# Kernel optimization log

Hardware: AMD Instinct MI355X
Metric: run time of the kernel (lower is better)

The kernel has to match this reference:

```python
import jax, jax.numpy as jnp
import numpy as np

B, T, D = 64, 2048, 256  # batch, seq_len, embedding_dim; units == embedding_dim == D
U = 256


def setup_inputs() -> dict:
    key = jax.random.key(0)
    ks = jax.random.split(key, 8)
    s = 1.0 / np.sqrt(D)
    return {
        "features": jax.random.normal(ks[0], (B, T, D), dtype=jnp.float32),
        "hidden": jax.random.normal(ks[1], (B, D), dtype=jnp.float32),
        "w1_w": jax.random.uniform(ks[2], (U, D), jnp.float32, -s, s),
        "w1_b": jax.random.uniform(ks[3], (U,), jnp.float32, -s, s),
        "w2_w": jax.random.uniform(ks[4], (U, D), jnp.float32, -s, s),
        "w2_b": jax.random.uniform(ks[5], (U,), jnp.float32, -s, s),
        "v_w": jax.random.uniform(ks[6], (1, U), jnp.float32, -s, s),
        "v_b": jax.random.uniform(ks[7], (1,), jnp.float32, -s, s),
    }


def reference(features, hidden, w1_w, w1_b, w2_w, w2_b, v_w, v_b):
    # features: [B, T, D], hidden: [B, D]
    proj = jnp.einsum('btd,ud->btu', features, w1_w) + w1_b  # w1(features)
    hid = jnp.einsum('bd,ud->bu', hidden, w2_w) + w2_b        # w2(hidden)
    score = jnp.einsum('btu,ou->bto', jnp.tanh(proj + hid[:, None, :]), v_w) + v_b  # [B,T,1]
    attn = jax.nn.softmax(score, axis=1)                      # [B,T,1]
    context = jnp.sum(attn * features, axis=1)                # [B,D]
    return context, attn
```

## Files before the change

### kernel.cpp

```cpp
#include <hip/hip_runtime.h>
#include <stdint.h>

#define Bq 64
#define Tq 2048
#define Dq 256
#define Uq 256
#define NTILE 32

typedef __bf16 bf16x8 __attribute__((ext_vector_type(8)));
typedef float f32x4 __attribute__((ext_vector_type(4)));

#define ASTR 1024
#define ABUF (4 * ASTR)
#define BSTR 4096
#define BBUF (4 * BSTR)

__device__ inline unsigned short rne_bf16(float a) {
  unsigned b = __float_as_uint(a);
  return (unsigned short)((b + 0x7FFFu + ((b >> 16) & 1u)) >> 16);
}

__device__ inline float fast_tanh(float x) {
  float e = __expf(2.0f * x);
  return 1.0f - 2.0f * __builtin_amdgcn_rcpf(e + 1.0f);
}

__global__ void k01_prep(const float* __restrict__ w1,
                         unsigned short* __restrict__ w1bf,
                         const float* __restrict__ hidden,
                         const float* __restrict__ w2_w,
                         const float* __restrict__ w2_b,
                         const float* __restrict__ w1_b,
                         float* __restrict__ comb) {
  if (blockIdx.x < 64) {
    int idx = blockIdx.x * 256 + threadIdx.x;
    int i = idx * 4;
    int u = i >> 8;
    int k = i & 255;
    float4 v = *reinterpret_cast<const float4*>(&w1[i]);
    ushort4 h;
    h.x = rne_bf16(v.x);
    h.y = rne_bf16(v.y);
    h.z = rne_bf16(v.z);
    h.w = rne_bf16(v.w);
    int dst = (k >> 3) * (Uq * 8) + u * 8 + (k & 7);
    *reinterpret_cast<ushort4*>(&w1bf[dst]) = h;
  } else {
    int bid = blockIdx.x - 64;
    int b = bid >> 6;
    int wave = threadIdx.x >> 6;
    int lane = threadIdx.x & 63;
    int u = (bid & 63) * 4 + wave;
    const float* h = hidden + b * Dq;
    const float* w = w2_w + u * Dq;
    float sum = 0.f;
#pragma unroll
    for (int i = 0; i < Dq; i += 64) sum += h[lane + i] * w[lane + i];
#pragma unroll
    for (int m = 32; m >= 1; m >>= 1) sum += __shfl_xor(sum, m, 64);
    if (lane == 0) comb[b * Uq + u] = sum + w2_b[u] + w1_b[u];
  }
}

__global__ __launch_bounds__(256) void k2_score(
    const float* __restrict__ feat, const unsigned short* __restrict__ w1bf,
    const float* __restrict__ comb, const float* __restrict__ v_w,
    const float* __restrict__ v_b, float* __restrict__ score,
    float* __restrict__ pm, float* __restrict__ partc) {
  __shared__ char sB[2 * BBUF];
  __shared__ char sA[2 * ABUF];
  float* const scp = reinterpret_cast<float*>(sA);
  float* const ebuf = reinterpret_cast<float*>(sA) + 256;
  const int b = blockIdx.y;
  const int tile = blockIdx.x;
  const int t0 = tile * 64;
  const int tid = threadIdx.x;
  const int w = tid >> 6;
  const int l = tid & 63;
  const int fr = l & 15;
  const int g = l >> 4;

  const int arow = tid >> 2;
  const int aoct = tid & 3;
  const float* aload = feat + ((size_t)(b * Tq + t0 + arow)) * Dq + aoct * 8;
  char* const awr = sA + aoct * ASTR + arow * 16;

  f32x4 acc[4][4] = {};
  float4 pa[2][2];

  auto issueBdma = [&](int c) {
    char* bbase = sB + (c & 1) * BBUF;
#pragma unroll
    for (int q = 0; q < 4; ++q) {
      int d = w * 4 + q;
      int j = d >> 2;
      int h2 = d & 3;
      const unsigned short* src =
          w1bf + (size_t)(c * 4 + j) * (Uq * 8) + (h2 * 64 + l) * 8;
      __builtin_amdgcn_global_load_lds(
          (const __attribute__((address_space(1))) unsigned int*)src,
          (__attribute__((address_space(3))) unsigned int*)(bbase + j * BSTR +
                                                            h2 * 1024),
          16, 0, 0);
    }
  };
  auto loadA = [&](int c) {
    pa[c & 1][0] = *reinterpret_cast<const float4*>(aload + c * 32);
    pa[c & 1][1] = *reinterpret_cast<const float4*>(aload + c * 32 + 4);
  };
  auto writeA = [&](int c) {
    const float4& v0 = pa[c & 1][0];
    const float4& v1 = pa[c & 1][1];
    uint4 H;
    H.x = rne_bf16(v0.x) | ((unsigned)rne_bf16(v0.y) << 16);
    H.y = rne_bf16(v0.z) | ((unsigned)rne_bf16(v0.w) << 16);
    H.z = rne_bf16(v1.x) | ((unsigned)rne_bf16(v1.y) << 16);
    H.w = rne_bf16(v1.z) | ((unsigned)rne_bf16(v1.w) << 16);
    *reinterpret_cast<uint4*>(awr + (c & 1) * ABUF) = H;
  };
  auto pipeBarrier = [&]() {
    __builtin_amdgcn_sched_barrier(0);
    asm volatile("s_waitcnt vmcnt(2) lgkmcnt(0)" ::: "memory");
    __builtin_amdgcn_s_barrier();
    __builtin_amdgcn_sched_barrier(0);
  };

  issueBdma(0);
  __builtin_amdgcn_sched_barrier(0);
  loadA(0);
  loadA(1);
  __builtin_amdgcn_sched_barrier(0);
  writeA(0);
  pipeBarrier();

#pragma unroll
  for (int c = 0; c < 8; ++c) {
    if (c < 7) {
      issueBdma(c + 1);
      __builtin_amdgcn_sched_barrier(0);
      loadA((c + 2) & 7);
      __builtin_amdgcn_sched_barrier(0);
    }
    const char* bA = sA + (c & 1) * ABUF;
    const char* bB = sB + (c & 1) * BBUF;
    bf16x8 ah[4], bh[4];
#pragma unroll
    for (int mf = 0; mf < 4; ++mf)
      ah[mf] = *reinterpret_cast<const bf16x8*>(bA + g * ASTR +
                                                (mf * 16 + fr) * 16);
#pragma unroll
    for (int nf = 0; nf < 4; ++nf)
      bh[nf] = *reinterpret_cast<const bf16x8*>(
          bB + g * BSTR + (w * 64 + nf * 16 + fr) * 16);
    __builtin_amdgcn_s_setprio(1);
#pragma unroll
    for (int mf = 0; mf < 4; ++mf)
#pragma unroll
      for (int nf = 0; nf < 4; ++nf)
        acc[mf][nf] = __builtin_amdgcn_mfma_f32_16x16x32_bf16(
            ah[mf], bh[nf], acc[mf][nf], 0, 0, 0);
    __builtin_amdgcn_s_setprio(0);
    if (c < 7) {
      writeA(c + 1);
      pipeBarrier();
    }
  }

  const float* frow = feat + (size_t)(b * Tq + t0) * Dq + tid;
  float fv0[16], fv1[16];
#pragma unroll
  for (int t = 0; t < 16; ++t) fv0[t] = frow[(size_t)t * Dq];
#pragma unroll
  for (int t = 0; t < 16; ++t) fv1[t] = frow[(size_t)(t + 16) * Dq];

  float cb[4], vw4[4];
#pragma unroll
  for (int nf = 0; nf < 4; ++nf) {
    int u = w * 64 + nf * 16 + fr;
    cb[nf] = comb[b * Uq + u];
    vw4[nf] = v_w[u];
  }
  float sc[4][4];
#pragma unroll
  for (int mf = 0; mf < 4; ++mf)
#pragma unroll
    for (int r = 0; r < 4; ++r) sc[mf][r] = 0.f;
#pragma unroll
  for (int mf = 0; mf < 4; ++mf)
#pragma unroll
    for (int nf = 0; nf < 4; ++nf)
#pragma unroll
      for (int r = 0; r < 4; ++r)
        sc[mf][r] += vw4[nf] * fast_tanh(acc[mf][nf][r] + cb[nf]);
#pragma unroll
  for (int m = 1; m < 16; m <<= 1)
#pragma unroll
    for (int mf = 0; mf < 4; ++mf)
#pragma unroll
      for (int r = 0; r < 4; ++r) sc[mf][r] += __shfl_xor(sc[mf][r], m, 16);
  __syncthreads();
  if (fr == 0) {
#pragma unroll
    for (int mf = 0; mf < 4; ++mf)
#pragma unroll
      for (int r = 0; r < 4; ++r)
        scp[w * 64 + mf * 16 + g * 4 + r] = sc[mf][r];
  }
  __syncthreads();
  if (tid < 64) {
    float v =
        scp[tid] + scp[64 + tid] + scp[128 + tid] + scp[192 + tid] + v_b[0];
    score[b * Tq + t0 + tid] = v;
    float m = v;
#pragma unroll
    for (int mk = 32; mk >= 1; mk >>= 1) m = fmaxf(m, __shfl_xor(m, mk, 64));
    ebuf[tid] = __expf(v - m);
    if (tid == 0) pm[b * NTILE + tile] = m;
  }
  __syncthreads();
  {
    float fv2[16], fv3[16];
#pragma unroll
    for (int t = 0; t < 16; ++t) fv2[t] = frow[(size_t)(t + 32) * Dq];
    float cd = 0.f;
#pragma unroll
    for (int t = 0; t < 16; ++t) cd += ebuf[t] * fv0[t];
#pragma unroll
    for (int t = 0; t < 16; ++t) fv3[t] = frow[(size_t)(t + 48) * Dq];
#pragma unroll
    for (int t = 0; t < 16; ++t) cd += ebuf[t + 16] * fv1[t];
#pragma unroll
    for (int t = 0; t < 16; ++t) cd += ebuf[t + 32] * fv2[t];
#pragma unroll
    for (int t = 0; t < 16; ++t) cd += ebuf[t + 48] * fv3[t];
    partc[((size_t)b * NTILE + tile) * Dq + tid] = cd;
  }
}

__global__ void k35_softmax_combine(float* __restrict__ s,
                                    const float* __restrict__ pm,
                                    const float* __restrict__ partc,
                                    float* __restrict__ ctx) {
  int b = blockIdx.x;
  int tid = threadIdx.x;
  const int base = b * Tq;
  float v[8];
  float m = -1e30f;
#pragma unroll
  for (int i = 0; i < 8; ++i) {
    v[i] = s[base + tid + 256 * i];
    m = fmaxf(m, v[i]);
  }
#pragma unroll
  for (int mk = 32; mk >= 1; mk >>= 1) m = fmaxf(m, __shfl_xor(m, mk, 64));
  __shared__ float red[4];
  int wv = tid >> 6, ln = tid & 63;
  if (ln == 0) red[wv] = m;
  __syncthreads();
  m = fmaxf(fmaxf(red[0], red[1]), fmaxf(red[2], red[3]));
  __syncthreads();
  float sum = 0.f;
#pragma unroll
  for (int i = 0; i < 8; ++i) {
    v[i] = __expf(v[i] - m);
    sum += v[i];
  }
#pragma unroll
  for (int mk = 32; mk >= 1; mk >>= 1) sum += __shfl_xor(sum, mk, 64);
  if (ln == 0) red[wv] = sum;
  __syncthreads();
  sum = red[0] + red[1] + red[2] + red[3];
  float inv = 1.f / sum;
#pragma unroll
  for (int i = 0; i < 8; ++i) s[base + tid + 256 * i] = v[i] * inv;

  __shared__ float wgt[NTILE];
  if (tid < NTILE) wgt[tid] = __expf(pm[b * NTILE + tid] - m);
  __syncthreads();
  float cs = 0.f;
#pragma unroll
  for (int j = 0; j < NTILE; ++j)
    cs += wgt[j] * partc[((size_t)b * NTILE + j) * Dq + tid];
  ctx[b * Dq + tid] = cs * inv;
}

extern "C" void kernel_launch(void* const* d_in, const int* in_sizes, int n_in,
                              void* d_out, int out_size, void* d_ws,
                              size_t ws_size, hipStream_t stream) {
  const float* feat   = (const float*)d_in[0];
  const float* hidden = (const float*)d_in[1];
  const float* w1_w   = (const float*)d_in[2];
  const float* w1_b   = (const float*)d_in[3];
  const float* w2_w   = (const float*)d_in[4];
  const float* w2_b   = (const float*)d_in[5];
  const float* v_w    = (const float*)d_in[6];
  const float* v_b    = (const float*)d_in[7];

  float* ctx  = (float*)d_out;
  float* attn = ctx + Bq * Dq;
  float* comb = (float*)d_ws;
  unsigned short* w1bf = (unsigned short*)(comb + Bq * Uq);
  float* partc = (float*)(w1bf + Uq * Dq);
  float* pm    = partc + (size_t)Bq * NTILE * Dq;

  k01_prep<<<64 + Bq * 64, 256, 0, stream>>>(w1_w, w1bf, hidden, w2_w, w2_b,
                                             w1_b, comb);
  k2_score<<<dim3(NTILE, Bq), 256, 0, stream>>>(feat, w1bf, comb, v_w, v_b,
                                                attn, pm, partc);
  k35_softmax_combine<<<Bq, 256, 0, stream>>>(attn, pm, partc, ctx);
}
```

Measured before the change: 61.76 us.

## Double score-kernel row tile to 128 with 512 threads sharing W1 tiles

Each block of the score kernel now covers 128 time steps instead of 64. It uses 8 waves in a 2x4 layout, so each bf16 W1 chunk staged in LDS serves two row groups, halving W1 reloads per token, and the grid shrinks to 16 tiles per batch. The A-tile LDS stride is padded to 2080 bytes, likely to reduce bank conflicts. The block-wide softmax max and the context partials are now combined across two halves through extra shared-memory reductions and barriers, which adds sync overhead and register pressure at 512 threads.

Result: slower. 65.63 us (+6.3%).

```diff
diff --git a/kernel.cpp b/kernel.cpp
--- a/kernel.cpp
+++ b/kernel.cpp
@@ -5,13 +5,13 @@
 #define Tq 2048
 #define Dq 256
 #define Uq 256
-#define NTILE 32
+#define NTILE 16
 
 typedef __bf16 bf16x8 __attribute__((ext_vector_type(8)));
 typedef float f32x4 __attribute__((ext_vector_type(4)));
 
-#define ASTR 1024
-#define ABUF (4 * ASTR)
+#define AOST 2080
+#define ABUF (4 * AOST)
 #define BSTR 4096
 #define BBUF (4 * BSTR)
 
@@ -62,7 +62,7 @@
   }
 }
 
-__global__ __launch_bounds__(256) void k2_score(
+__global__ __launch_bounds__(512) void k2_score(
     const float* __restrict__ feat, const unsigned short* __restrict__ w1bf,
     const float* __restrict__ comb, const float* __restrict__ v_w,
     const float* __restrict__ v_b, float* __restrict__ score,
@@ -70,20 +70,24 @@
   __shared__ char sB[2 * BBUF];
   __shared__ char sA[2 * ABUF];
   float* const scp = reinterpret_cast<float*>(sA);
-  float* const ebuf = reinterpret_cast<float*>(sA) + 256;
+  float* const ebuf = reinterpret_cast<float*>(sA) + 512;
+  float* const red = reinterpret_cast<float*>(sA) + 640;
+  float* const cbuf = reinterpret_cast<float*>(sA) + 644;
   const int b = blockIdx.y;
   const int tile = blockIdx.x;
-  const int t0 = tile * 64;
+  const int t0 = tile * 128;
   const int tid = threadIdx.x;
   const int w = tid >> 6;
   const int l = tid & 63;
   const int fr = l & 15;
   const int g = l >> 4;
+  const int wr = w >> 2;
+  const int wc = w & 3;
 
   const int arow = tid >> 2;
   const int aoct = tid & 3;
   const float* aload = feat + ((size_t)(b * Tq + t0 + arow)) * Dq + aoct * 8;
-  char* const awr = sA + aoct * ASTR + arow * 16;
+  char* const awr = sA + aoct * AOST + arow * 16;
 
   f32x4 acc[4][4] = {};
   float4 pa[2][2];
@@ -91,8 +95,8 @@
   auto issueBdma = [&](int c) {
     char* bbase = sB + (c & 1) * BBUF;
 #pragma unroll
-    for (int q = 0; q < 4; ++q) {
-      int d = w * 4 + q;
+    for (int q = 0; q < 2; ++q) {
+      int d = w * 2 + q;
       int j = d >> 2;
       int h2 = d & 3;
       const unsigned short* src =
@@ -146,12 +150,12 @@
     bf16x8 ah[4], bh[4];
 #pragma unroll
     for (int mf = 0; mf < 4; ++mf)
-      ah[mf] = *reinterpret_cast<const bf16x8*>(bA + g * ASTR +
-                                                (mf * 16 + fr) * 16);
+      ah[mf] = *reinterpret_cast<const bf16x8*>(
+          bA + g * AOST + (wr * 64 + mf * 16 + fr) * 16);
 #pragma unroll
     for (int nf = 0; nf < 4; ++nf)
       bh[nf] = *reinterpret_cast<const bf16x8*>(
-          bB + g * BSTR + (w * 64 + nf * 16 + fr) * 16);
+          bB + g * BSTR + (wc * 64 + nf * 16 + fr) * 16);
     __builtin_amdgcn_s_setprio(1);
 #pragma unroll
     for (int mf = 0; mf < 4; ++mf)
@@ -166,7 +170,10 @@
     }
   }
 
-  const float* frow = feat + (size_t)(b * Tq + t0) * Dq + tid;
+  const int cd_ = tid & 255;
+  const int th = tid >> 8;
+  const float* frow =
+      feat + ((size_t)(b * Tq + t0 + th * 64)) * Dq + cd_;
   float fv0[16], fv1[16];
 #pragma unroll
   for (int t = 0; t < 16; ++t) fv0[t] = frow[(size_t)t * Dq];
@@ -176,7 +183,7 @@
   float cb[4], vw4[4];
 #pragma unroll
   for (int nf = 0; nf < 4; ++nf) {
-    int u = w * 64 + nf * 16 + fr;
+    int u = wc * 64 + nf * 16 + fr;
     cb[nf] = comb[b * Uq + u];
     vw4[nf] = v_w[u];
   }
@@ -204,36 +211,44 @@
     for (int mf = 0; mf < 4; ++mf)
 #pragma unroll
       for (int r = 0; r < 4; ++r)
-        scp[w * 64 + mf * 16 + g * 4 + r] = sc[mf][r];
-  }
-  __syncthreads();
-  if (tid < 64) {
-    float v =
-        scp[tid] + scp[64 + tid] + scp[128 + tid] + scp[192 + tid] + v_b[0];
+        scp[wc * 128 + wr * 64 + mf * 16 + g * 4 + r] = sc[mf][r];
+  }
+  __syncthreads();
+  float v = 0.f;
+  if (tid < 128) {
+    v = scp[tid] + scp[128 + tid] + scp[256 + tid] + scp[384 + tid] + v_b[0];
     score[b * Tq + t0 + tid] = v;
-    float m = v;
-#pragma unroll
-    for (int mk = 32; mk >= 1; mk >>= 1) m = fmaxf(m, __shfl_xor(m, mk, 64));
-    ebuf[tid] = __expf(v - m);
-    if (tid == 0) pm[b * NTILE + tile] = m;
-  }
+    float mloc = v;
+#pragma unroll
+    for (int mk = 32; mk >= 1; mk >>= 1)
+      mloc = fmaxf(mloc, __shfl_xor(mloc, mk, 64));
+    if ((tid & 63) == 0) red[tid >> 6] = mloc;
+  }
+  __syncthreads();
+  const float mb = fmaxf(red[0], red[1]);
+  if (tid < 128) ebuf[tid] = __expf(v - mb);
+  if (tid == 0) pm[b * NTILE + tile] = mb;
   __syncthreads();
   {
+    const float* eb = ebuf + th * 64;
     float fv2[16], fv3[16];
 #pragma unroll
     for (int t = 0; t < 16; ++t) fv2[t] = frow[(size_t)(t + 32) * Dq];
     float cd = 0.f;
 #pragma unroll
-    for (int t = 0; t < 16; ++t) cd += ebuf[t] * fv0[t];
+    for (int t = 0; t < 16; ++t) cd += eb[t] * fv0[t];
 #pragma unroll
     for (int t = 0; t < 16; ++t) fv3[t] = frow[(size_t)(t + 48) * Dq];
 #pragma unroll
-    for (int t = 0; t < 16; ++t) cd += ebuf[t + 16] * fv1[t];
-#pragma unroll
-    for (int t = 0; t < 16; ++t) cd += ebuf[t + 32] * fv2[t];
-#pragma unroll
-    for (int t = 0; t < 16; ++t) cd += ebuf[t + 48] * fv3[t];
-    partc[((size_t)b * NTILE + tile) * Dq + tid] = cd;
+    for (int t = 0; t < 16; ++t) cd += eb[t + 16] * fv1[t];
+#pragma unroll
+    for (int t = 0; t < 16; ++t) cd += eb[t + 32] * fv2[t];
+#pragma unroll
+    for (int t = 0; t < 16; ++t) cd += eb[t + 48] * fv3[t];
+    if (th == 1) cbuf[cd_] = cd;
+    __syncthreads();
+    if (th == 0)
+      partc[((size_t)b * NTILE + tile) * Dq + cd_] = cd + cbuf[cd_];
   }
 }
 
@@ -305,7 +320,7 @@
 
   k01_prep<<<64 + Bq * 64, 256, 0, stream>>>(w1_w, w1bf, hidden, w2_w, w2_b,
                                              w1_b, comb);
-  k2_score<<<dim3(NTILE, Bq), 256, 0, stream>>>(feat, w1bf, comb, v_w, v_b,
+  k2_score<<<dim3(NTILE, Bq), 512, 0, stream>>>(feat, w1bf, comb, v_w, v_b,
                                                 attn, pm, partc);
   k35_softmax_combine<<<Bq, 256, 0, stream>>>(attn, pm, partc, ctx);
 }
```
